# Kernel tuning notes

Hardware: AMD Instinct MI355X
Metric: run time of the kernel (lower is better)

Reference implementation:

```python
import jax, jax.numpy as jnp
import numpy as np

N_NODES = 100000
N_EDGES = 800000
D = 32           # output_dim == node feature dim
D_EDGE = 32      # embedded edge feature dim
H = 64           # psi hidden units
PSI_IN = 4 * D + D_EDGE  # 160


def setup_inputs() -> dict:
    key = jax.random.key(0)
    ks = jax.random.split(key, 12)
    inp = {
        "h_d_prev": jax.random.normal(ks[0], (N_NODES, D), dtype=jnp.float32),
        "h_s": jax.random.normal(ks[1], (N_NODES, D), dtype=jnp.float32),
        "edge_features_embedded": jax.random.normal(ks[2], (N_EDGES, D_EDGE), dtype=jnp.float32),
        "sender_indices": jax.random.randint(ks[3], (N_EDGES,), 0, N_NODES, dtype=jnp.int32),
        "receiver_indices": jax.random.randint(ks[4], (N_EDGES,), 0, N_NODES, dtype=jnp.int32),
        # psi MLP params (Dense with relu on every layer, incl. last since final_activation=None)
        "psi_w0": jax.random.normal(ks[5], (PSI_IN, H), dtype=jnp.float32) * (1.0 / np.sqrt(PSI_IN)),
        "psi_b0": jnp.zeros((H,), dtype=jnp.float32),
        "psi_w1": jax.random.normal(ks[6], (H, H), dtype=jnp.float32) * (1.0 / np.sqrt(H)),
        "psi_b1": jnp.zeros((H,), dtype=jnp.float32),
        "psi_w2": jax.random.normal(ks[7], (H, D), dtype=jnp.float32) * (1.0 / np.sqrt(H)),
        "psi_b2": jnp.zeros((D,), dtype=jnp.float32),
        # final W matrix (Dense, no bias)
        "W": jax.random.normal(ks[8], (D, D), dtype=jnp.float32) * (1.0 / np.sqrt(D)),
    }
    return inp


def reference(h_d_prev, h_s, edge_features_embedded, sender_indices, receiver_indices,
              psi_w0, psi_b0, psi_w1, psi_b1, psi_w2, psi_b2, W):
    # Gather node features onto edges
    h_di = h_d_prev[sender_indices]      # [E, D]
    h_dj = h_d_prev[receiver_indices]    # [E, D]
    h_si = h_s[sender_indices]           # [E, D]
    h_sj = h_s[receiver_indices]         # [E, D]

    psi_in = jnp.concatenate([h_si, h_sj, h_di, h_dj, edge_features_embedded], axis=-1)  # [E, 4D+De]
    x = jax.nn.relu(psi_in @ psi_w0 + psi_b0)
    x = jax.nn.relu(x @ psi_w1 + psi_b1)
    psi_out = jax.nn.relu(x @ psi_w2 + psi_b2)  # [E, D]

    s_ij = psi_out * (h_dj - h_di)  # [E, D]
    aggregated = jax.ops.segment_sum(s_ij, receiver_indices, num_segments=h_d_prev.shape[0])  # [N, D]
    return h_d_prev + aggregated @ W
```

## Files before the change

### kernel.cpp

```cpp
#include <hip/hip_runtime.h>

#define DD 32
#define HH 64

#define XSTR 72
#define DSTR 35

typedef __attribute__((ext_vector_type(8))) short bf16x8;
typedef __attribute__((ext_vector_type(4))) float f32x4;

static __device__ __forceinline__ unsigned short f2bf(float x) {
    union { float f; unsigned u; } v; v.f = x;
    unsigned r = (v.u + 0x7FFFu + ((v.u >> 16) & 1u)) >> 16;
    return (unsigned short)r;
}

static __device__ __forceinline__ float bf2f(unsigned short x) {
    union { unsigned u; float f; } v; v.u = ((unsigned)x) << 16;
    return v.f;
}

__global__ __launch_bounds__(256) void prep_weights(
    const float* __restrict__ w0, const float* __restrict__ w1,
    const float* __restrict__ w2, unsigned short* __restrict__ frags)
{
    const int tid = blockIdx.x * 256 + threadIdx.x;
    const int f = tid >> 6, l = tid & 63;
    if (f >= 32) return;
    const int c = l & 15, q = l >> 4;
    unsigned short* dst = frags + f * 512 + l * 8;
    if (f < 20) {
        const int kk = f >> 2, t = f & 3;
        const int n = t * 16 + c, kb = kk * 32 + q * 8;
        #pragma unroll
        for (int j = 0; j < 8; ++j) dst[j] = f2bf(w0[(kb + j) * HH + n]);
    } else if (f < 28) {
        const int f2 = f - 20, kk = f2 >> 2, t = f2 & 3;
        const int n = t * 16 + c, kb = kk * 32 + q * 8;
        #pragma unroll
        for (int j = 0; j < 8; ++j) dst[j] = f2bf(w1[(kb + j) * HH + n]);
    } else {
        const int f3 = f - 28, kk = f3 >> 1, t = f3 & 1;
        const int n = t * 16 + c, kb = kk * 32 + q * 8;
        #pragma unroll
        for (int j = 0; j < 8; ++j) dst[j] = f2bf(w2[(kb + j) * DD + n]);
    }
}

__global__ __launch_bounds__(256) void pack_nodes(
    const float* __restrict__ h_d, const float* __restrict__ h_s,
    unsigned short* __restrict__ npack, int N)
{
    const int tid = blockIdx.x * 256 + threadIdx.x;
    if (tid >= N * 8) return;
    const int n = tid >> 3, chunk = tid & 7;
    const float* src = (chunk < 4) ? (h_s + (size_t)n * DD + chunk * 8)
                                   : (h_d + (size_t)n * DD + (chunk - 4) * 8);
    const float4 v0 = ((const float4*)src)[0];
    const float4 v1 = ((const float4*)src)[1];
    unsigned short* dst = npack + (size_t)n * 64 + chunk * 8;
    dst[0] = f2bf(v0.x); dst[1] = f2bf(v0.y); dst[2] = f2bf(v0.z); dst[3] = f2bf(v0.w);
    dst[4] = f2bf(v1.x); dst[5] = f2bf(v1.y); dst[6] = f2bf(v1.z); dst[7] = f2bf(v1.w);
}

__global__ __launch_bounds__(512, 4) void edge_mfma(
    const unsigned short* __restrict__ npack,
    const float* __restrict__ ef,
    const int* __restrict__ snd, const int* __restrict__ rcv,
    const unsigned short* __restrict__ frags,
    const float* __restrict__ b0, const float* __restrict__ b1,
    const float* __restrict__ b2,
    float* __restrict__ agg, int E, int ntiles)
{
    __shared__ __align__(16) unsigned short wlds[20 * 512];
    __shared__ __align__(16) unsigned short xbuf[8][16 * XSTR];
    __shared__ float hdiff[8][16 * DSTR];
    __shared__ int rcvb[8][16];

    const int lane = threadIdx.x & 63;
    const int w = threadIdx.x >> 6;
    const int c = lane & 15, q = lane >> 4;

    for (int i = threadIdx.x; i < 20 * 512 / 8; i += 512)
        ((float4*)wlds)[i] = ((const float4*)frags)[i];
    bf16x8 wf1[8], wf2[4];
    #pragma unroll
    for (int t = 0; t < 8; ++t)
        wf1[t] = *(const bf16x8*)(frags + (20 + t) * 512 + lane * 8);
    #pragma unroll
    for (int t = 0; t < 4; ++t)
        wf2[t] = *(const bf16x8*)(frags + (28 + t) * 512 + lane * 8);
    __syncthreads();

    const float b0t[4] = {b0[c], b0[16 + c], b0[32 + c], b0[48 + c]};
    const float b1t[4] = {b1[c], b1[16 + c], b1[32 + c], b1[48 + c]};
    const float b2t[2] = {b2[c], b2[16 + c]};

    unsigned short* xb = xbuf[w];
    float* hd = hdiff[w];
    int* rb = rcvb[w];

    const int wave_id = blockIdx.x * 8 + w;
    const int nwaves = gridDim.x * 8;

    int nsi = 0, nri = 0;
    if (wave_id < ntiles) {
        int e0 = wave_id * 16 + c; if (e0 >= E) e0 = E - 1;
        nsi = __builtin_nontemporal_load(snd + e0);
        nri = __builtin_nontemporal_load(rcv + e0);
    }

    for (int tile = wave_id; tile < ntiles; tile += nwaves) {
        const int base = tile * 16;
        const int si = nsi, ri = nri;
        {
            const int nt = tile + nwaves;
            if (nt < ntiles) {
                int e2 = nt * 16 + c; if (e2 >= E) e2 = E - 1;
                nsi = __builtin_nontemporal_load(snd + e2);
                nri = __builtin_nontemporal_load(rcv + e2);
            }
        }
        int e = base + c; if (e >= E) e = E - 1;

        const unsigned short* nps = npack + (size_t)si * 64 + q * 8;
        const unsigned short* npr = npack + (size_t)ri * 64 + q * 8;
        const bf16x8 a_ss = *(const bf16x8*)nps;
        const bf16x8 a_sr = *(const bf16x8*)npr;
        const bf16x8 a_ds = *(const bf16x8*)(nps + 32);
        const bf16x8 a_dr = *(const bf16x8*)(npr + 32);
        const f32x4 e0v = __builtin_nontemporal_load((const f32x4*)(ef + (size_t)e * DD + q * 8));
        const f32x4 e1v = __builtin_nontemporal_load((const f32x4*)(ef + (size_t)e * DD + q * 8) + 1);

        #pragma unroll
        for (int j = 0; j < 8; ++j)
            hd[c * DSTR + q * 8 + j] =
                bf2f((unsigned short)a_dr[j]) - bf2f((unsigned short)a_ds[j]);
        if (q == 0) rb[c] = ri;

        bf16x8 aef;
        aef[0] = (short)f2bf(e0v[0]); aef[1] = (short)f2bf(e0v[1]);
        aef[2] = (short)f2bf(e0v[2]); aef[3] = (short)f2bf(e0v[3]);
        aef[4] = (short)f2bf(e1v[0]); aef[5] = (short)f2bf(e1v[1]);
        aef[6] = (short)f2bf(e1v[2]); aef[7] = (short)f2bf(e1v[3]);

        const bf16x8 af[5] = {a_ss, a_sr, a_ds, a_dr, aef};
        f32x4 c0[4] = {f32x4{0,0,0,0}, f32x4{0,0,0,0}, f32x4{0,0,0,0}, f32x4{0,0,0,0}};
        #pragma unroll
        for (int kk = 0; kk < 5; ++kk) {
            #pragma unroll
            for (int t = 0; t < 4; ++t) {
                const bf16x8 b = *(const bf16x8*)(wlds + (kk * 4 + t) * 512 + lane * 8);
                c0[t] = __builtin_amdgcn_mfma_f32_16x16x32_bf16(af[kk], b, c0[t], 0, 0, 0);
            }
        }
        #pragma unroll
        for (int t = 0; t < 4; ++t) {
            #pragma unroll
            for (int r = 0; r < 4; ++r) {
                const float v = fmaxf(c0[t][r] + b0t[t], 0.0f);
                xb[(q * 4 + r) * XSTR + t * 16 + c] = f2bf(v);
            }
        }

        f32x4 c1[4] = {f32x4{0,0,0,0}, f32x4{0,0,0,0}, f32x4{0,0,0,0}, f32x4{0,0,0,0}};
        #pragma unroll
        for (int kk = 0; kk < 2; ++kk) {
            const bf16x8 a = *(const bf16x8*)(xb + c * XSTR + kk * 32 + q * 8);
            #pragma unroll
            for (int t = 0; t < 4; ++t)
                c1[t] = __builtin_amdgcn_mfma_f32_16x16x32_bf16(a, wf1[kk * 4 + t], c1[t], 0, 0, 0);
        }
        #pragma unroll
        for (int t = 0; t < 4; ++t) {
            #pragma unroll
            for (int r = 0; r < 4; ++r) {
                const float v = fmaxf(c1[t][r] + b1t[t], 0.0f);
                xb[(q * 4 + r) * XSTR + t * 16 + c] = f2bf(v);
            }
        }

        f32x4 c2[2] = {f32x4{0,0,0,0}, f32x4{0,0,0,0}};
        #pragma unroll
        for (int kk = 0; kk < 2; ++kk) {
            const bf16x8 a = *(const bf16x8*)(xb + c * XSTR + kk * 32 + q * 8);
            #pragma unroll
            for (int t = 0; t < 2; ++t)
                c2[t] = __builtin_amdgcn_mfma_f32_16x16x32_bf16(a, wf2[kk * 2 + t], c2[t], 0, 0, 0);
        }

        int rir[4];
        #pragma unroll
        for (int r = 0; r < 4; ++r) rir[r] = rb[q * 4 + r];
        #pragma unroll
        for (int t = 0; t < 2; ++t) {
            const int h = t * 16 + c;
            #pragma unroll
            for (int r = 0; r < 4; ++r) {
                const int ee = base + q * 4 + r;
                if (ee < E) {
                    const float psi = fmaxf(c2[t][r] + b2t[t], 0.0f);
                    const float d = hd[(q * 4 + r) * DSTR + h];
                    atomicAdd(agg + (size_t)rir[r] * DD + h, psi * d);
                }
            }
        }
    }
}

__global__ __launch_bounds__(256) void out_kernel(
    const float* __restrict__ h_d, const float* __restrict__ agg,
    const float* __restrict__ W, float* __restrict__ out, int N)
{
    const int idx = blockIdx.x * 256 + threadIdx.x;
    if (idx >= N * DD) return;
    const int n = idx >> 5;
    const int d = idx & 31;
    const float* arow = agg + (size_t)n * DD;
    float s = h_d[idx];
    #pragma unroll
    for (int k = 0; k < DD; ++k) s = fmaf(arow[k], W[k * DD + d], s);
    out[idx] = s;
}

extern "C" void kernel_launch(void* const* d_in, const int* in_sizes, int n_in,
                              void* d_out, int out_size, void* d_ws, size_t ws_size,
                              hipStream_t stream) {
    const float* h_d = (const float*)d_in[0];
    const float* h_s = (const float*)d_in[1];
    const float* ef  = (const float*)d_in[2];
    const int*   snd = (const int*)d_in[3];
    const int*   rcv = (const int*)d_in[4];
    const float* w0  = (const float*)d_in[5];
    const float* b0  = (const float*)d_in[6];
    const float* w1  = (const float*)d_in[7];
    const float* b1  = (const float*)d_in[8];
    const float* w2  = (const float*)d_in[9];
    const float* b2  = (const float*)d_in[10];
    const float* W   = (const float*)d_in[11];
    float* out = (float*)d_out;

    const int N = in_sizes[0] / DD;
    const int E = in_sizes[3];
    const int ntiles = (E + 15) / 16;

    float* agg = (float*)d_ws;
    unsigned short* frags = (unsigned short*)((char*)d_ws + (size_t)N * DD * sizeof(float));
    unsigned short* npack = frags + 32 * 512;

    hipMemsetAsync(agg, 0, (size_t)N * DD * sizeof(float), stream);
    prep_weights<<<8, 256, 0, stream>>>(w0, w1, w2, frags);
    pack_nodes<<<(N * 8 + 255) / 256, 256, 0, stream>>>(h_d, h_s, npack, N);
    edge_mfma<<<512, 512, 0, stream>>>(npack, ef, snd, rcv, frags,
                                       b0, b1, b2, agg, E, ntiles);
    out_kernel<<<((N * DD) + 255) / 256, 256, 0, stream>>>(h_d, agg, W, out, N);
}
```

Baseline: 410.2 us.

## Sort edges by receiver via counting sort before the edge MFMA kernel

Adds histogram, single-block scan and scatter kernels that bucket edges by receiver index, producing permuted sender/receiver arrays and a permutation into edge features. The edge kernel then walks contiguous tile ranges per wave, so receiver-node gathers and the atomic adds into the aggregate land on nearby, repeated addresses. Edge-feature reads become a gather through the permutation. The extra passes add cost, including a slow single-block scan over 100k nodes, and the next-tile index prefetch is dropped. The LDS stride for the difference buffer also changes.

```diff
diff --git a/kernel.cpp b/kernel.cpp
--- a/kernel.cpp
+++ b/kernel.cpp
@@ -4,7 +4,7 @@
 #define HH 64
 
 #define XSTR 72
-#define DSTR 35
+#define DSTR 33
 
 typedef __attribute__((ext_vector_type(8))) short bf16x8;
 typedef __attribute__((ext_vector_type(4))) float f32x4;
@@ -63,10 +63,52 @@
     dst[4] = f2bf(v1.x); dst[5] = f2bf(v1.y); dst[6] = f2bf(v1.z); dst[7] = f2bf(v1.w);
 }
 
+__global__ __launch_bounds__(256) void hist_kernel(
+    const int* __restrict__ rcv, int* __restrict__ cnt, int E)
+{
+    const int i = blockIdx.x * 256 + threadIdx.x;
+    if (i < E) atomicAdd(cnt + rcv[i], 1);
+}
+
+__global__ __launch_bounds__(1024) void scan_kernel(int* __restrict__ cnt, int n)
+{
+    __shared__ int sums[1024];
+    const int t = threadIdx.x;
+    const int chunk = (n + 1023) >> 10;
+    const int lo = t * chunk;
+    const int hi = (lo + chunk < n) ? lo + chunk : n;
+    int s = 0;
+    for (int i = lo; i < hi; ++i) s += cnt[i];
+    sums[t] = s;
+    __syncthreads();
+    for (int d = 1; d < 1024; d <<= 1) {
+        int v = (t >= d) ? sums[t - d] : 0;
+        __syncthreads();
+        sums[t] += v;
+        __syncthreads();
+    }
+    int run = (t > 0) ? sums[t - 1] : 0;
+    for (int i = lo; i < hi; ++i) { const int old = cnt[i]; cnt[i] = run; run += old; }
+}
+
+__global__ __launch_bounds__(256) void scatter_kernel(
+    const int* __restrict__ snd, const int* __restrict__ rcv, int* __restrict__ cnt,
+    int* __restrict__ perm, int* __restrict__ snd_s, int* __restrict__ rcv_s, int E)
+{
+    const int i = blockIdx.x * 256 + threadIdx.x;
+    if (i >= E) return;
+    const int r = rcv[i];
+    const int pos = atomicAdd(cnt + r, 1);
+    perm[pos] = i;
+    snd_s[pos] = snd[i];
+    rcv_s[pos] = r;
+}
+
 __global__ __launch_bounds__(512, 4) void edge_mfma(
     const unsigned short* __restrict__ npack,
     const float* __restrict__ ef,
-    const int* __restrict__ snd, const int* __restrict__ rcv,
+    const int* __restrict__ perm,
+    const int* __restrict__ snd_s, const int* __restrict__ rcv_s,
     const unsigned short* __restrict__ frags,
     const float* __restrict__ b0, const float* __restrict__ b1,
     const float* __restrict__ b2,
@@ -75,7 +117,6 @@
     __shared__ __align__(16) unsigned short wlds[20 * 512];
     __shared__ __align__(16) unsigned short xbuf[8][16 * XSTR];
     __shared__ float hdiff[8][16 * DSTR];
-    __shared__ int rcvb[8][16];
 
     const int lane = threadIdx.x & 63;
     const int w = threadIdx.x >> 6;
@@ -98,30 +139,19 @@
 
     unsigned short* xb = xbuf[w];
     float* hd = hdiff[w];
-    int* rb = rcvb[w];
 
     const int wave_id = blockIdx.x * 8 + w;
     const int nwaves = gridDim.x * 8;
-
-    int nsi = 0, nri = 0;
-    if (wave_id < ntiles) {
-        int e0 = wave_id * 16 + c; if (e0 >= E) e0 = E - 1;
-        nsi = __builtin_nontemporal_load(snd + e0);
-        nri = __builtin_nontemporal_load(rcv + e0);
-    }
-
-    for (int tile = wave_id; tile < ntiles; tile += nwaves) {
+    const int per = (ntiles + nwaves - 1) / nwaves;
+    const int tile0 = wave_id * per;
+    const int tile1 = (tile0 + per < ntiles) ? tile0 + per : ntiles;
+
+    for (int tile = tile0; tile < tile1; ++tile) {
         const int base = tile * 16;
-        const int si = nsi, ri = nri;
-        {
-            const int nt = tile + nwaves;
-            if (nt < ntiles) {
-                int e2 = nt * 16 + c; if (e2 >= E) e2 = E - 1;
-                nsi = __builtin_nontemporal_load(snd + e2);
-                nri = __builtin_nontemporal_load(rcv + e2);
-            }
-        }
-        int e = base + c; if (e >= E) e = E - 1;
+        int p = base + c; if (p >= E) p = E - 1;
+        const int si = snd_s[p];
+        const int ri = rcv_s[p];
+        const int ee = perm[p];
 
         const unsigned short* nps = npack + (size_t)si * 64 + q * 8;
         const unsigned short* npr = npack + (size_t)ri * 64 + q * 8;
@@ -129,14 +159,13 @@
         const bf16x8 a_sr = *(const bf16x8*)npr;
         const bf16x8 a_ds = *(const bf16x8*)(nps + 32);
         const bf16x8 a_dr = *(const bf16x8*)(npr + 32);
-        const f32x4 e0v = __builtin_nontemporal_load((const f32x4*)(ef + (size_t)e * DD + q * 8));
-        const f32x4 e1v = __builtin_nontemporal_load((const f32x4*)(ef + (size_t)e * DD + q * 8) + 1);
+        const f32x4 e0v = __builtin_nontemporal_load((const f32x4*)(ef + (size_t)ee * DD + q * 8));
+        const f32x4 e1v = __builtin_nontemporal_load((const f32x4*)(ef + (size_t)ee * DD + q * 8) + 1);
 
         #pragma unroll
         for (int j = 0; j < 8; ++j)
             hd[c * DSTR + q * 8 + j] =
                 bf2f((unsigned short)a_dr[j]) - bf2f((unsigned short)a_ds[j]);
-        if (q == 0) rb[c] = ri;
 
         bf16x8 aef;
         aef[0] = (short)f2bf(e0v[0]); aef[1] = (short)f2bf(e0v[1]);
@@ -189,16 +218,15 @@
                 c2[t] = __builtin_amdgcn_mfma_f32_16x16x32_bf16(a, wf2[kk * 2 + t], c2[t], 0, 0, 0);
         }
 
-        int rir[4];
-        #pragma unroll
-        for (int r = 0; r < 4; ++r) rir[r] = rb[q * 4 + r];
+        const int4 rr4 = *(const int4*)(rcv_s + base + q * 4);
+        const int rir[4] = {rr4.x, rr4.y, rr4.z, rr4.w};
         #pragma unroll
         for (int t = 0; t < 2; ++t) {
             const int h = t * 16 + c;
             #pragma unroll
             for (int r = 0; r < 4; ++r) {
-                const int ee = base + q * 4 + r;
-                if (ee < E) {
+                const int pp = base + q * 4 + r;
+                if (pp < E) {
                     const float psi = fmaxf(c2[t][r] + b2t[t], 0.0f);
                     const float d = hd[(q * 4 + r) * DSTR + h];
                     atomicAdd(agg + (size_t)rir[r] * DD + h, psi * d);
@@ -244,14 +272,27 @@
     const int E = in_sizes[3];
     const int ntiles = (E + 15) / 16;
 
-    float* agg = (float*)d_ws;
-    unsigned short* frags = (unsigned short*)((char*)d_ws + (size_t)N * DD * sizeof(float));
-    unsigned short* npack = frags + 32 * 512;
+    char* ws = (char*)d_ws;
+    size_t off = 0;
+    auto walloc = [&](size_t bytes) {
+        char* ptr = ws + off; off += (bytes + 255) & ~(size_t)255; return ptr;
+    };
+    float* agg            = (float*)walloc((size_t)N * DD * sizeof(float));
+    unsigned short* frags = (unsigned short*)walloc(32 * 512 * sizeof(unsigned short));
+    unsigned short* npack = (unsigned short*)walloc((size_t)N * 64 * sizeof(unsigned short));
+    int* cnt              = (int*)walloc((size_t)(N + 1) * sizeof(int));
+    int* perm             = (int*)walloc((size_t)E * sizeof(int));
+    int* snd_s            = (int*)walloc((size_t)E * sizeof(int));
+    int* rcv_s            = (int*)walloc((size_t)(E + 16) * sizeof(int));
 
     hipMemsetAsync(agg, 0, (size_t)N * DD * sizeof(float), stream);
+    hipMemsetAsync(cnt, 0, (size_t)(N + 1) * sizeof(int), stream);
     prep_weights<<<8, 256, 0, stream>>>(w0, w1, w2, frags);
     pack_nodes<<<(N * 8 + 255) / 256, 256, 0, stream>>>(h_d, h_s, npack, N);
-    edge_mfma<<<512, 512, 0, stream>>>(npack, ef, snd, rcv, frags,
+    hist_kernel<<<(E + 255) / 256, 256, 0, stream>>>(rcv, cnt, E);
+    scan_kernel<<<1, 1024, 0, stream>>>(cnt, N);
+    scatter_kernel<<<(E + 255) / 256, 256, 0, stream>>>(snd, rcv, cnt, perm, snd_s, rcv_s, E);
+    edge_mfma<<<512, 512, 0, stream>>>(npack, ef, perm, snd_s, rcv_s, frags,
                                        b0, b1, b2, agg, E, ntiles);
     out_kernel<<<((N * DD) + 255) / 256, 256, 0, stream>>>(h_d, agg, W, out, N);
 }
```

Measured after the change: 795.8 us. 94.0% more time.

## Replace float atomics with receiver-sorted CSR gather aggregation fused with output

Applied to the files above, without the earlier changes.

Builds a receiver histogram, prefix scan and permutation so edges can be grouped by receiver. The edge MLP kernel now writes per-edge messages as bf16 to a buffer. A new kernel gathers each node's messages through the permutation and applies the W projection plus residual in one pass. This removes the 25.6M float atomicAdds and the separate aggregation buffer. In exchange it adds several extra kernels, an E×32 intermediate write and read, integer atomics for the histogram and scatter, and bf16 rounding of messages before summation. The old atomic path is kept as a fallback when workspace is too small.

```diff
diff --git a/kernel.cpp b/kernel.cpp
--- a/kernel.cpp
+++ b/kernel.cpp
@@ -4,7 +4,7 @@
 #define HH 64
 
 #define XSTR 72
-#define DSTR 35
+#define DSTR 33
 
 typedef __attribute__((ext_vector_type(8))) short bf16x8;
 typedef __attribute__((ext_vector_type(4))) float f32x4;
@@ -47,35 +47,77 @@
     }
 }
 
-__global__ __launch_bounds__(256) void pack_nodes(
+__global__ __launch_bounds__(256) void pack_hist(
     const float* __restrict__ h_d, const float* __restrict__ h_s,
-    unsigned short* __restrict__ npack, int N)
+    unsigned short* __restrict__ npack,
+    const int* __restrict__ rcv, int* __restrict__ cnt, int N, int E)
 {
     const int tid = blockIdx.x * 256 + threadIdx.x;
-    if (tid >= N * 8) return;
-    const int n = tid >> 3, chunk = tid & 7;
-    const float* src = (chunk < 4) ? (h_s + (size_t)n * DD + chunk * 8)
-                                   : (h_d + (size_t)n * DD + (chunk - 4) * 8);
-    const float4 v0 = ((const float4*)src)[0];
-    const float4 v1 = ((const float4*)src)[1];
-    unsigned short* dst = npack + (size_t)n * 64 + chunk * 8;
-    dst[0] = f2bf(v0.x); dst[1] = f2bf(v0.y); dst[2] = f2bf(v0.z); dst[3] = f2bf(v0.w);
-    dst[4] = f2bf(v1.x); dst[5] = f2bf(v1.y); dst[6] = f2bf(v1.z); dst[7] = f2bf(v1.w);
-}
-
-__global__ __launch_bounds__(512, 4) void edge_mfma(
+    if (tid < N * 8) {
+        const int n = tid >> 3, chunk = tid & 7;
+        const float* src = (chunk < 4) ? (h_s + (size_t)n * DD + chunk * 8)
+                                       : (h_d + (size_t)n * DD + (chunk - 4) * 8);
+        const float4 v0 = ((const float4*)src)[0];
+        const float4 v1 = ((const float4*)src)[1];
+        unsigned short* dst = npack + (size_t)n * 64 + chunk * 8;
+        dst[0] = f2bf(v0.x); dst[1] = f2bf(v0.y); dst[2] = f2bf(v0.z); dst[3] = f2bf(v0.w);
+        dst[4] = f2bf(v1.x); dst[5] = f2bf(v1.y); dst[6] = f2bf(v1.z); dst[7] = f2bf(v1.w);
+    }
+    if (cnt != nullptr && tid < E) atomicAdd(cnt + rcv[tid], 1);
+}
+
+__global__ __launch_bounds__(1024) void scan1(int* __restrict__ cnt, int* __restrict__ btot, int N)
+{
+    __shared__ int s[1024];
+    const int t = threadIdx.x;
+    const int i = blockIdx.x * 1024 + t;
+    const int v = (i < N) ? cnt[i] : 0;
+    s[t] = v; __syncthreads();
+    for (int d = 1; d < 1024; d <<= 1) {
+        const int x = (t >= d) ? s[t - d] : 0;
+        __syncthreads(); s[t] += x; __syncthreads();
+    }
+    if (i < N) cnt[i] = s[t] - v;
+    if (t == 1023) btot[blockIdx.x] = s[1023];
+}
+
+__global__ __launch_bounds__(128) void scan2(
+    const int* __restrict__ btot, int* __restrict__ boffs, int nb)
+{
+    __shared__ int s[128];
+    const int t = threadIdx.x;
+    const int v = (t < nb) ? btot[t] : 0;
+    s[t] = v; __syncthreads();
+    for (int d = 1; d < 128; d <<= 1) {
+        const int x = (t >= d) ? s[t - d] : 0;
+        __syncthreads(); s[t] += x; __syncthreads();
+    }
+    if (t < nb) boffs[t] = s[t] - v;
+}
+
+__global__ __launch_bounds__(256) void scatter_perm(
+    const int* __restrict__ rcv, int* __restrict__ cnt, const int* __restrict__ boffs,
+    int* __restrict__ perm, int E)
+{
+    const int i = blockIdx.x * 256 + threadIdx.x;
+    if (i >= E) return;
+    const int r = rcv[i];
+    const int pos = atomicAdd(cnt + r, 1) + boffs[r >> 10];
+    perm[pos] = i;
+}
+
+__global__ __launch_bounds__(512, 4) void edge_psi(
     const unsigned short* __restrict__ npack,
     const float* __restrict__ ef,
     const int* __restrict__ snd, const int* __restrict__ rcv,
     const unsigned short* __restrict__ frags,
     const float* __restrict__ b0, const float* __restrict__ b1,
     const float* __restrict__ b2,
-    float* __restrict__ agg, int E, int ntiles)
+    unsigned short* __restrict__ sij, int E, int ntiles)
 {
     __shared__ __align__(16) unsigned short wlds[20 * 512];
     __shared__ __align__(16) unsigned short xbuf[8][16 * XSTR];
     __shared__ float hdiff[8][16 * DSTR];
-    __shared__ int rcvb[8][16];
 
     const int lane = threadIdx.x & 63;
     const int w = threadIdx.x >> 6;
@@ -98,7 +140,6 @@
 
     unsigned short* xb = xbuf[w];
     float* hd = hdiff[w];
-    int* rb = rcvb[w];
 
     const int wave_id = blockIdx.x * 8 + w;
     const int nwaves = gridDim.x * 8;
@@ -136,7 +177,6 @@
         for (int j = 0; j < 8; ++j)
             hd[c * DSTR + q * 8 + j] =
                 bf2f((unsigned short)a_dr[j]) - bf2f((unsigned short)a_ds[j]);
-        if (q == 0) rb[c] = ri;
 
         bf16x8 aef;
         aef[0] = (short)f2bf(e0v[0]); aef[1] = (short)f2bf(e0v[1]);
@@ -189,6 +229,189 @@
                 c2[t] = __builtin_amdgcn_mfma_f32_16x16x32_bf16(a, wf2[kk * 2 + t], c2[t], 0, 0, 0);
         }
 
+        #pragma unroll
+        for (int t = 0; t < 2; ++t) {
+            #pragma unroll
+            for (int r = 0; r < 4; ++r) {
+                const float psi = fmaxf(c2[t][r] + b2t[t], 0.0f);
+                const float v = psi * hd[(q * 4 + r) * DSTR + t * 16 + c];
+                xb[(q * 4 + r) * XSTR + t * 16 + c] = f2bf(v);
+            }
+        }
+        const int eo = base + c;
+        if (eo < E && q < 4) {
+            const f32x4 vv = *(const f32x4*)(xb + c * XSTR + q * 8);
+            __builtin_nontemporal_store(vv, (f32x4*)(sij + (size_t)eo * DD + q * 8));
+        }
+    }
+}
+
+__global__ __launch_bounds__(256) void aggregate_out(
+    const unsigned short* __restrict__ sij,
+    const int* __restrict__ perm,
+    const int* __restrict__ cnt, const int* __restrict__ boffs,
+    const float* __restrict__ h_d, const float* __restrict__ W,
+    float* __restrict__ out, int N)
+{
+    __shared__ float Wl[32 * 32];
+    __shared__ float accT[4][4][33];
+    const int t = threadIdx.x;
+    for (int i = t; i < 1024; i += 256) Wl[i] = W[i];
+    __syncthreads();
+
+    const int w = t >> 6, lane = t & 63;
+    const int ni = lane >> 4, d = lane & 15;
+    const int n = blockIdx.x * 16 + w * 4 + ni;
+    if (n >= N) return;
+
+    const int start = (n == 0) ? 0 : (cnt[n - 1] + boffs[(n - 1) >> 10]);
+    const int end = cnt[n] + boffs[n >> 10];
+
+    float ax = 0.0f, ay = 0.0f;
+    for (int j = start; j < end; ++j) {
+        const int p = perm[j];
+        const unsigned pv = *(const unsigned*)(sij + (size_t)p * DD + 2 * d);
+        ax += bf2f((unsigned short)(pv & 0xffffu));
+        ay += bf2f((unsigned short)(pv >> 16));
+    }
+    float* at = &accT[w][ni][0];
+    at[2 * d] = ax; at[2 * d + 1] = ay;
+
+    const float2 hv = *(const float2*)(h_d + (size_t)n * DD + 2 * d);
+    float ox = hv.x, oy = hv.y;
+    #pragma unroll
+    for (int k = 0; k < 32; ++k) {
+        const float a = at[k];
+        ox += a * Wl[k * 32 + 2 * d];
+        oy += a * Wl[k * 32 + 2 * d + 1];
+    }
+    float2 ov; ov.x = ox; ov.y = oy;
+    *(float2*)(out + (size_t)n * DD + 2 * d) = ov;
+}
+
+__global__ __launch_bounds__(512, 4) void edge_atomic(
+    const unsigned short* __restrict__ npack,
+    const float* __restrict__ ef,
+    const int* __restrict__ snd, const int* __restrict__ rcv,
+    const unsigned short* __restrict__ frags,
+    const float* __restrict__ b0, const float* __restrict__ b1,
+    const float* __restrict__ b2,
+    float* __restrict__ agg, int E, int ntiles)
+{
+    __shared__ __align__(16) unsigned short wlds[20 * 512];
+    __shared__ __align__(16) unsigned short xbuf[8][16 * XSTR];
+    __shared__ float hdiff[8][16 * DSTR];
+    __shared__ int rcvb[8][16];
+
+    const int lane = threadIdx.x & 63;
+    const int w = threadIdx.x >> 6;
+    const int c = lane & 15, q = lane >> 4;
+
+    for (int i = threadIdx.x; i < 20 * 512 / 8; i += 512)
+        ((float4*)wlds)[i] = ((const float4*)frags)[i];
+    bf16x8 wf1[8], wf2[4];
+    #pragma unroll
+    for (int t = 0; t < 8; ++t)
+        wf1[t] = *(const bf16x8*)(frags + (20 + t) * 512 + lane * 8);
+    #pragma unroll
+    for (int t = 0; t < 4; ++t)
+        wf2[t] = *(const bf16x8*)(frags + (28 + t) * 512 + lane * 8);
+    __syncthreads();
+
+    const float b0t[4] = {b0[c], b0[16 + c], b0[32 + c], b0[48 + c]};
+    const float b1t[4] = {b1[c], b1[16 + c], b1[32 + c], b1[48 + c]};
+    const float b2t[2] = {b2[c], b2[16 + c]};
+
+    unsigned short* xb = xbuf[w];
+    float* hd = hdiff[w];
+    int* rb = rcvb[w];
+
+    const int wave_id = blockIdx.x * 8 + w;
+    const int nwaves = gridDim.x * 8;
+
+    int nsi = 0, nri = 0;
+    if (wave_id < ntiles) {
+        int e0 = wave_id * 16 + c; if (e0 >= E) e0 = E - 1;
+        nsi = __builtin_nontemporal_load(snd + e0);
+        nri = __builtin_nontemporal_load(rcv + e0);
+    }
+
+    for (int tile = wave_id; tile < ntiles; tile += nwaves) {
+        const int base = tile * 16;
+        const int si = nsi, ri = nri;
+        {
+            const int nt = tile + nwaves;
+            if (nt < ntiles) {
+                int e2 = nt * 16 + c; if (e2 >= E) e2 = E - 1;
+                nsi = __builtin_nontemporal_load(snd + e2);
+                nri = __builtin_nontemporal_load(rcv + e2);
+            }
+        }
+        int e = base + c; if (e >= E) e = E - 1;
+
+        const unsigned short* nps = npack + (size_t)si * 64 + q * 8;
+        const unsigned short* npr = npack + (size_t)ri * 64 + q * 8;
+        const bf16x8 a_ss = *(const bf16x8*)nps;
+        const bf16x8 a_sr = *(const bf16x8*)npr;
+        const bf16x8 a_ds = *(const bf16x8*)(nps + 32);
+        const bf16x8 a_dr = *(const bf16x8*)(npr + 32);
+        const f32x4 e0v = __builtin_nontemporal_load((const f32x4*)(ef + (size_t)e * DD + q * 8));
+        const f32x4 e1v = __builtin_nontemporal_load((const f32x4*)(ef + (size_t)e * DD + q * 8) + 1);
+
+        #pragma unroll
+        for (int j = 0; j < 8; ++j)
+            hd[c * DSTR + q * 8 + j] =
+                bf2f((unsigned short)a_dr[j]) - bf2f((unsigned short)a_ds[j]);
+        if (q == 0) rb[c] = ri;
+
+        bf16x8 aef;
+        aef[0] = (short)f2bf(e0v[0]); aef[1] = (short)f2bf(e0v[1]);
+        aef[2] = (short)f2bf(e0v[2]); aef[3] = (short)f2bf(e0v[3]);
+        aef[4] = (short)f2bf(e1v[0]); aef[5] = (short)f2bf(e1v[1]);
+        aef[6] = (short)f2bf(e1v[2]); aef[7] = (short)f2bf(e1v[3]);
+
+        const bf16x8 af[5] = {a_ss, a_sr, a_ds, a_dr, aef};
+        f32x4 c0[4] = {f32x4{0,0,0,0}, f32x4{0,0,0,0}, f32x4{0,0,0,0}, f32x4{0,0,0,0}};
+        #pragma unroll
+        for (int kk = 0; kk < 5; ++kk) {
+            #pragma unroll
+            for (int t = 0; t < 4; ++t) {
+                const bf16x8 b = *(const bf16x8*)(wlds + (kk * 4 + t) * 512 + lane * 8);
+                c0[t] = __builtin_amdgcn_mfma_f32_16x16x32_bf16(af[kk], b, c0[t], 0, 0, 0);
+            }
+        }
+        #pragma unroll
+        for (int t = 0; t < 4; ++t) {
+            #pragma unroll
+            for (int r = 0; r < 4; ++r) {
+                const float v = fmaxf(c0[t][r] + b0t[t], 0.0f);
+                xb[(q * 4 + r) * XSTR + t * 16 + c] = f2bf(v);
+            }
+        }
+        f32x4 c1[4] = {f32x4{0,0,0,0}, f32x4{0,0,0,0}, f32x4{0,0,0,0}, f32x4{0,0,0,0}};
+        #pragma unroll
+        for (int kk = 0; kk < 2; ++kk) {
+            const bf16x8 a = *(const bf16x8*)(xb + c * XSTR + kk * 32 + q * 8);
+            #pragma unroll
+            for (int t = 0; t < 4; ++t)
+                c1[t] = __builtin_amdgcn_mfma_f32_16x16x32_bf16(a, wf1[kk * 4 + t], c1[t], 0, 0, 0);
+        }
+        #pragma unroll
+        for (int t = 0; t < 4; ++t) {
+            #pragma unroll
+            for (int r = 0; r < 4; ++r) {
+                const float v = fmaxf(c1[t][r] + b1t[t], 0.0f);
+                xb[(q * 4 + r) * XSTR + t * 16 + c] = f2bf(v);
+            }
+        }
+        f32x4 c2[2] = {f32x4{0,0,0,0}, f32x4{0,0,0,0}};
+        #pragma unroll
+        for (int kk = 0; kk < 2; ++kk) {
+            const bf16x8 a = *(const bf16x8*)(xb + c * XSTR + kk * 32 + q * 8);
+            #pragma unroll
+            for (int t = 0; t < 2; ++t)
+                c2[t] = __builtin_amdgcn_mfma_f32_16x16x32_bf16(a, wf2[kk * 2 + t], c2[t], 0, 0, 0);
+        }
         int rir[4];
         #pragma unroll
         for (int r = 0; r < 4; ++r) rir[r] = rb[q * 4 + r];
@@ -243,15 +466,40 @@
     const int N = in_sizes[0] / DD;
     const int E = in_sizes[3];
     const int ntiles = (E + 15) / 16;
-
-    float* agg = (float*)d_ws;
-    unsigned short* frags = (unsigned short*)((char*)d_ws + (size_t)N * DD * sizeof(float));
-    unsigned short* npack = frags + 32 * 512;
-
-    hipMemsetAsync(agg, 0, (size_t)N * DD * sizeof(float), stream);
-    prep_weights<<<8, 256, 0, stream>>>(w0, w1, w2, frags);
-    pack_nodes<<<(N * 8 + 255) / 256, 256, 0, stream>>>(h_d, h_s, npack, N);
-    edge_mfma<<<512, 512, 0, stream>>>(npack, ef, snd, rcv, frags,
-                                       b0, b1, b2, agg, E, ntiles);
-    out_kernel<<<((N * DD) + 255) / 256, 256, 0, stream>>>(h_d, agg, W, out, N);
-}
+    const int nb = (N + 1023) / 1024;
+
+    char* ws = (char*)d_ws;
+    size_t off = 0;
+    auto walloc = [&](size_t bytes) {
+        char* ptr = ws + off; off += (bytes + 255) & ~(size_t)255; return ptr;
+    };
+    unsigned short* frags = (unsigned short*)walloc(32 * 512 * sizeof(unsigned short));
+    unsigned short* npack = (unsigned short*)walloc((size_t)N * 64 * sizeof(unsigned short));
+    int* cnt              = (int*)walloc((size_t)N * sizeof(int));
+    int* btot             = (int*)walloc(128 * sizeof(int));
+    int* boffs            = (int*)walloc(128 * sizeof(int));
+    int* perm             = (int*)walloc((size_t)E * sizeof(int));
+    const size_t need_main = off + (((size_t)E * DD * sizeof(unsigned short) + 255) & ~(size_t)255);
+
+    if (need_main <= ws_size) {
+        unsigned short* sij = (unsigned short*)walloc((size_t)E * DD * sizeof(unsigned short));
+        (void)hipMemsetAsync(cnt, 0, (size_t)N * sizeof(int), stream);
+        prep_weights<<<8, 256, 0, stream>>>(w0, w1, w2, frags);
+        pack_hist<<<(N * 8 + 255) / 256, 256, 0, stream>>>(h_d, h_s, npack, rcv, cnt, N, E);
+        scan1<<<nb, 1024, 0, stream>>>(cnt, btot, N);
+        scan2<<<1, 128, 0, stream>>>(btot, boffs, nb);
+        scatter_perm<<<(E + 255) / 256, 256, 0, stream>>>(rcv, cnt, boffs, perm, E);
+        edge_psi<<<512, 512, 0, stream>>>(npack, ef, snd, rcv, frags,
+                                          b0, b1, b2, sij, E, ntiles);
+        aggregate_out<<<(N + 15) / 16, 256, 0, stream>>>(sij, perm, cnt, boffs,
+                                                         h_d, W, out, N);
+    } else {
+        float* agg = (float*)walloc((size_t)N * DD * sizeof(float));
+        (void)hipMemsetAsync(agg, 0, (size_t)N * DD * sizeof(float), stream);
+        prep_weights<<<8, 256, 0, stream>>>(w0, w1, w2, frags);
+        pack_hist<<<(N * 8 + 255) / 256, 256, 0, stream>>>(h_d, h_s, npack, rcv, nullptr, N, E);
+        edge_atomic<<<512, 512, 0, stream>>>(npack, ef, snd, rcv, frags,
+                                             b0, b1, b2, agg, E, ntiles);
+        out_kernel<<<((N * DD) + 255) / 256, 256, 0, stream>>>(h_d, agg, W, out, N);
+    }
+}
```

Result: slower. 497.2 us (+21.2%).

## Cut registers and LDS in edge MLP kernel to raise occupancy

Applied to the files above, without the earlier changes.

The layer-1 weight fragments move from registers into LDS, the hidden-activation buffer uses an XOR swizzle instead of padding, the h_d difference is stored as bf16 instead of fp32, and receiver indices are fetched with a wave shuffle instead of an LDS array. These cuts in register and LDS use allow launch bounds of 6 blocks per CU and a grid of 768 blocks instead of 512, aiming to hide gather and atomic latency. In exchange, each tile does more LDS reads for the weights, and rounding the difference to bf16 adds some precision loss.

```diff
diff --git a/kernel.cpp b/kernel.cpp
--- a/kernel.cpp
+++ b/kernel.cpp
@@ -3,8 +3,7 @@
 #define DD 32
 #define HH 64
 
-#define XSTR 72
-#define DSTR 35
+#define HSTR 36
 
 typedef __attribute__((ext_vector_type(8))) short bf16x8;
 typedef __attribute__((ext_vector_type(4))) float f32x4;
@@ -63,7 +62,7 @@
     dst[4] = f2bf(v1.x); dst[5] = f2bf(v1.y); dst[6] = f2bf(v1.z); dst[7] = f2bf(v1.w);
 }
 
-__global__ __launch_bounds__(512, 4) void edge_mfma(
+__global__ __launch_bounds__(512, 6) void edge_mfma(
     const unsigned short* __restrict__ npack,
     const float* __restrict__ ef,
     const int* __restrict__ snd, const int* __restrict__ rcv,
@@ -72,21 +71,17 @@
     const float* __restrict__ b2,
     float* __restrict__ agg, int E, int ntiles)
 {
-    __shared__ __align__(16) unsigned short wlds[20 * 512];
-    __shared__ __align__(16) unsigned short xbuf[8][16 * XSTR];
-    __shared__ float hdiff[8][16 * DSTR];
-    __shared__ int rcvb[8][16];
+    __shared__ __align__(16) unsigned short wlds[28 * 512];
+    __shared__ __align__(16) unsigned short xbuf[8][16 * 64];
+    __shared__ __align__(16) unsigned short hdiff[8][16 * HSTR];
 
     const int lane = threadIdx.x & 63;
     const int w = threadIdx.x >> 6;
     const int c = lane & 15, q = lane >> 4;
 
-    for (int i = threadIdx.x; i < 20 * 512 / 8; i += 512)
+    for (int i = threadIdx.x; i < 28 * 512 / 8; i += 512)
         ((float4*)wlds)[i] = ((const float4*)frags)[i];
-    bf16x8 wf1[8], wf2[4];
-    #pragma unroll
-    for (int t = 0; t < 8; ++t)
-        wf1[t] = *(const bf16x8*)(frags + (20 + t) * 512 + lane * 8);
+    bf16x8 wf2[4];
     #pragma unroll
     for (int t = 0; t < 4; ++t)
         wf2[t] = *(const bf16x8*)(frags + (28 + t) * 512 + lane * 8);
@@ -97,8 +92,7 @@
     const float b2t[2] = {b2[c], b2[16 + c]};
 
     unsigned short* xb = xbuf[w];
-    float* hd = hdiff[w];
-    int* rb = rcvb[w];
+    unsigned short* hd = hdiff[w];
 
     const int wave_id = blockIdx.x * 8 + w;
     const int nwaves = gridDim.x * 8;
@@ -133,10 +127,10 @@
         const f32x4 e1v = __builtin_nontemporal_load((const f32x4*)(ef + (size_t)e * DD + q * 8) + 1);
 
         #pragma unroll
-        for (int j = 0; j < 8; ++j)
-            hd[c * DSTR + q * 8 + j] =
-                bf2f((unsigned short)a_dr[j]) - bf2f((unsigned short)a_ds[j]);
-        if (q == 0) rb[c] = ri;
+        for (int j = 0; j < 8; ++j) {
+            const float dv = bf2f((unsigned short)a_dr[j]) - bf2f((unsigned short)a_ds[j]);
+            hd[c * HSTR + q * 8 + j] = f2bf(dv);
+        }
 
         bf16x8 aef;
         aef[0] = (short)f2bf(e0v[0]); aef[1] = (short)f2bf(e0v[1]);
@@ -159,31 +153,35 @@
             #pragma unroll
             for (int r = 0; r < 4; ++r) {
                 const float v = fmaxf(c0[t][r] + b0t[t], 0.0f);
-                xb[(q * 4 + r) * XSTR + t * 16 + c] = f2bf(v);
+                const int row = q * 4 + r;
+                xb[(row * 64 + t * 16 + c) ^ ((row & 7) << 3)] = f2bf(v);
             }
         }
 
         f32x4 c1[4] = {f32x4{0,0,0,0}, f32x4{0,0,0,0}, f32x4{0,0,0,0}, f32x4{0,0,0,0}};
         #pragma unroll
         for (int kk = 0; kk < 2; ++kk) {
-            const bf16x8 a = *(const bf16x8*)(xb + c * XSTR + kk * 32 + q * 8);
-            #pragma unroll
-            for (int t = 0; t < 4; ++t)
-                c1[t] = __builtin_amdgcn_mfma_f32_16x16x32_bf16(a, wf1[kk * 4 + t], c1[t], 0, 0, 0);
+            const bf16x8 a = *(const bf16x8*)(xb + ((c * 64 + kk * 32 + q * 8) ^ ((c & 7) << 3)));
+            #pragma unroll
+            for (int t = 0; t < 4; ++t) {
+                const bf16x8 b = *(const bf16x8*)(wlds + (20 + kk * 4 + t) * 512 + lane * 8);
+                c1[t] = __builtin_amdgcn_mfma_f32_16x16x32_bf16(a, b, c1[t], 0, 0, 0);
+            }
         }
         #pragma unroll
         for (int t = 0; t < 4; ++t) {
             #pragma unroll
             for (int r = 0; r < 4; ++r) {
                 const float v = fmaxf(c1[t][r] + b1t[t], 0.0f);
-                xb[(q * 4 + r) * XSTR + t * 16 + c] = f2bf(v);
+                const int row = q * 4 + r;
+                xb[(row * 64 + t * 16 + c) ^ ((row & 7) << 3)] = f2bf(v);
             }
         }
 
         f32x4 c2[2] = {f32x4{0,0,0,0}, f32x4{0,0,0,0}};
         #pragma unroll
         for (int kk = 0; kk < 2; ++kk) {
-            const bf16x8 a = *(const bf16x8*)(xb + c * XSTR + kk * 32 + q * 8);
+            const bf16x8 a = *(const bf16x8*)(xb + ((c * 64 + kk * 32 + q * 8) ^ ((c & 7) << 3)));
             #pragma unroll
             for (int t = 0; t < 2; ++t)
                 c2[t] = __builtin_amdgcn_mfma_f32_16x16x32_bf16(a, wf2[kk * 2 + t], c2[t], 0, 0, 0);
@@ -191,7 +189,7 @@
 
         int rir[4];
         #pragma unroll
-        for (int r = 0; r < 4; ++r) rir[r] = rb[q * 4 + r];
+        for (int r = 0; r < 4; ++r) rir[r] = __shfl(ri, q * 4 + r);
         #pragma unroll
         for (int t = 0; t < 2; ++t) {
             const int h = t * 16 + c;
@@ -200,7 +198,7 @@
                 const int ee = base + q * 4 + r;
                 if (ee < E) {
                     const float psi = fmaxf(c2[t][r] + b2t[t], 0.0f);
-                    const float d = hd[(q * 4 + r) * DSTR + h];
+                    const float d = bf2f(hd[(q * 4 + r) * HSTR + h]);
                     atomicAdd(agg + (size_t)rir[r] * DD + h, psi * d);
                 }
             }
@@ -244,14 +242,19 @@
     const int E = in_sizes[3];
     const int ntiles = (E + 15) / 16;
 
-    float* agg = (float*)d_ws;
-    unsigned short* frags = (unsigned short*)((char*)d_ws + (size_t)N * DD * sizeof(float));
-    unsigned short* npack = frags + 32 * 512;
-
-    hipMemsetAsync(agg, 0, (size_t)N * DD * sizeof(float), stream);
+    char* ws = (char*)d_ws;
+    size_t off = 0;
+    auto walloc = [&](size_t bytes) {
+        char* ptr = ws + off; off += (bytes + 255) & ~(size_t)255; return ptr;
+    };
+    float* agg            = (float*)walloc((size_t)N * DD * sizeof(float));
+    unsigned short* frags = (unsigned short*)walloc(32 * 512 * sizeof(unsigned short));
+    unsigned short* npack = (unsigned short*)walloc((size_t)N * 64 * sizeof(unsigned short));
+
+    (void)hipMemsetAsync(agg, 0, (size_t)N * DD * sizeof(float), stream);
     prep_weights<<<8, 256, 0, stream>>>(w0, w1, w2, frags);
     pack_nodes<<<(N * 8 + 255) / 256, 256, 0, stream>>>(h_d, h_s, npack, N);
-    edge_mfma<<<512, 512, 0, stream>>>(npack, ef, snd, rcv, frags,
+    edge_mfma<<<768, 512, 0, stream>>>(npack, ef, snd, rcv, frags,
                                        b0, b1, b2, agg, E, ntiles);
     out_kernel<<<((N * DD) + 255) / 256, 256, 0, stream>>>(h_d, agg, W, out, N);
 }
```

Result: slower. 615.2 us (+50.0%).
